# Performance work log

Measured on AMD Instinct MI355X. Metric: run time of the kernel, lower is better.

Reference implementation:

```python
import jax, jax.numpy as jnp
import numpy as np

N_NODES = 100000
N_EDGES = 800000
IN_DIM, HID_DIM, OUT_DIM = 128, 256, 128


def setup_inputs() -> dict:
    key = jax.random.key(0)
    ks = jax.random.split(key, 8)
    x = jax.random.normal(ks[0], (N_NODES, IN_DIM), dtype=jnp.float32)
    edge_index = jax.random.randint(ks[1], (2, N_EDGES), 0, N_NODES, dtype=jnp.int32)
    s = lambda k, shp, fan_in: jax.random.normal(k, shp, dtype=jnp.float32) / np.sqrt(fan_in)
    return {
        "x": x,
        "edge_index": edge_index,
        "W1_l": s(ks[2], (HID_DIM, IN_DIM), IN_DIM),   # applied to aggregated neighbors
        "b1": jnp.zeros((HID_DIM,), jnp.float32),
        "W1_r": s(ks[3], (HID_DIM, IN_DIM), IN_DIM),   # root/self transform (no bias, as in PyG)
        "W2_l": s(ks[4], (OUT_DIM, HID_DIM), HID_DIM),
        "b2": jnp.zeros((OUT_DIM,), jnp.float32),
        "W2_r": s(ks[5], (OUT_DIM, HID_DIM), HID_DIM),
    }


def _sage_conv(x, src, dst, W_l, b, W_r):
    # mean aggregation of source-neighbor features onto targets
    msg = x[src]                                              # [E, d]
    agg = jax.ops.segment_sum(msg, dst, num_segments=N_NODES)  # [N, d]
    cnt = jax.ops.segment_sum(jnp.ones((src.shape[0],), x.dtype), dst, num_segments=N_NODES)
    mean = agg / jnp.maximum(cnt, 1.0)[:, None]
    # SAGEConv: lin_l(aggr) + lin_r(x)
    return mean @ W_l.T + b + x @ W_r.T


def reference(x, edge_index, W1_l, b1, W1_r, W2_l, b2, W2_r):
    src, dst = edge_index[0], edge_index[1]
    h = jax.nn.relu(_sage_conv(x, src, dst, W1_l, b1, W1_r))
    # dropout p=0.0 -> identity (eval-mode equivalent)
    out = _sage_conv(h, src, dst, W2_l, b2, W2_r)
    return out
```

## Files before the change

kernel.cpp:

```cpp
#include <hip/hip_runtime.h>

#define NN 100000
#define NE 800000

typedef __attribute__((ext_vector_type(4))) float f32x4;
typedef __attribute__((ext_vector_type(4))) int   i32x4;
typedef __attribute__((ext_vector_type(8))) unsigned short u16x8;

__device__ __forceinline__ unsigned short f2bf(float f) {
  unsigned u = __float_as_uint(f);
  return (unsigned short)((u + 0x7FFFu + ((u >> 16) & 1u)) >> 16);
}
__device__ __forceinline__ float bf2f(unsigned short b) {
  return __uint_as_float(((unsigned)b) << 16);
}

#define NBDEG 3125
#define NXV   (NN * 128 / 4)
#define NBX   12500
#define NBW   512
__global__ __launch_bounds__(256) void prep_k(
    const float* __restrict__ x,
    const float* __restrict__ Wa, const float* __restrict__ Wbm,
    const float* __restrict__ Wc, const float* __restrict__ Wd,
    const int* __restrict__ dst,
    unsigned short* __restrict__ xb, unsigned short* __restrict__ Wbo,
    int* __restrict__ deg, int* __restrict__ rord) {
  int bid = blockIdx.x, t = threadIdx.x;
  if (bid < NBDEG) {
    int e = bid * 256 + t;
    int o = atomicAdd(&deg[dst[e]], 1);
    __builtin_nontemporal_store(o, &rord[e]);
  } else if (bid < NBDEG + NBX) {
    int i = (bid - NBDEG) * 256 + t;
    float4 v = *reinterpret_cast<const float4*>(x + (size_t)i * 4);
    ushort4 o;
    o.x = f2bf(v.x); o.y = f2bf(v.y); o.z = f2bf(v.z); o.w = f2bf(v.w);
    *reinterpret_cast<ushort4*>(xb + (size_t)i * 4) = o;
  } else {
    int k = (bid - NBDEG - NBX) * 256 + t;
    int seg = k >> 15, off = k & 32767;
    const float* s = (seg < 2) ? (seg == 0 ? Wa : Wbm) : (seg == 2 ? Wc : Wd);
    Wbo[k] = f2bf(s[off]);
  }
}

__global__ __launch_bounds__(256) void scan1_k(const int* __restrict__ deg,
    int* __restrict__ offs, int* __restrict__ bsum, float* __restrict__ inv) {
  __shared__ int s[256];
  int t = threadIdx.x;
  int base = blockIdx.x * 1024 + t * 4;
  int v[4], tsum = 0;
#pragma unroll
  for (int k = 0; k < 4; ++k) {
    int i = base + k;
    v[k] = (i < NN) ? deg[i] : 0;
    tsum += v[k];
    if (i < NN) inv[i] = 1.0f / fmaxf((float)v[k], 1.0f);
  }
  s[t] = tsum; __syncthreads();
  int val = tsum;
#pragma unroll
  for (int off = 1; off < 256; off <<= 1) {
    int x = (t >= off) ? s[t - off] : 0;
    __syncthreads();
    val += x; s[t] = val;
    __syncthreads();
  }
  int excl = val - tsum;
  if (t == 255) bsum[blockIdx.x] = val;
  int run = excl;
#pragma unroll
  for (int k = 0; k < 4; ++k) { int i = base + k; if (i < NN) offs[i] = run; run += v[k]; }
}

__global__ __launch_bounds__(256) void scan2_k(int* __restrict__ bsum, int nb) {
  __shared__ int s[256];
  int t = threadIdx.x;
  int v = (t < nb) ? bsum[t] : 0;
  s[t] = v; __syncthreads();
  int val = v;
#pragma unroll
  for (int off = 1; off < 256; off <<= 1) {
    int x = (t >= off) ? s[t - off] : 0;
    __syncthreads();
    val += x; s[t] = val;
    __syncthreads();
  }
  if (t < nb) bsum[t] = val - v;
}

#define NBFIN 98
__global__ __launch_bounds__(256) void finfill_k(
    const int* __restrict__ offs, const int* __restrict__ bsum,
    int* __restrict__ offs2,
    const int* __restrict__ src, const int* __restrict__ dst,
    const int* __restrict__ rord, int* __restrict__ eidx) {
  int bid = blockIdx.x, t = threadIdx.x;
  if (bid < NBFIN) {
    int base = bid * 1024 + t * 4;
    int add = bsum[bid];
#pragma unroll
    for (int k = 0; k < 4; ++k) {
      int i = base + k;
      if (i < NN) offs2[i] = offs[i] + add;
    }
  } else {
    int e = (bid - NBFIN) * 256 + t;
    if (e < NE) {
      int d = dst[e];
      int p = offs[d] + bsum[d >> 10] + rord[e];
      __builtin_nontemporal_store(src[e], &eidx[p]);
    }
  }
}

template<int GMODE>
__global__ __launch_bounds__(256) void gather_k(const unsigned short* __restrict__ feat,
    const int* __restrict__ offs, const int* __restrict__ deg,
    const float* __restrict__ inv, const int* __restrict__ eidx,
    const unsigned short* __restrict__ selfb,
    unsigned short* __restrict__ outb, float* __restrict__ outf) {
  const int l = threadIdx.x & 15;
  for (int nb = blockIdx.x * 16; nb < NN; nb += gridDim.x * 16) {
    int node = nb + (threadIdx.x >> 4);
    if (node >= NN) continue;
    int st = offs[node], n = deg[node];
    float a[8];
#pragma unroll
    for (int k = 0; k < 8; ++k) a[k] = 0.f;

    int j = 0;
    for (; j + 8 <= n; j += 8) {
      int si[8];
#pragma unroll
      for (int q = 0; q < 8; ++q) si[q] = eidx[st + j + q];
      u16x8 r[8];
#pragma unroll
      for (int q = 0; q < 8; ++q)
        r[q] = *reinterpret_cast<const u16x8*>(feat + (size_t)si[q] * 128 + l * 8);
#pragma unroll
      for (int q = 0; q < 8; ++q)
#pragma unroll
        for (int k = 0; k < 8; ++k) a[k] += bf2f(r[q][k]);
    }
    for (; j + 4 <= n; j += 4) {
      int si[4];
#pragma unroll
      for (int q = 0; q < 4; ++q) si[q] = eidx[st + j + q];
      u16x8 r[4];
#pragma unroll
      for (int q = 0; q < 4; ++q)
        r[q] = *reinterpret_cast<const u16x8*>(feat + (size_t)si[q] * 128 + l * 8);
#pragma unroll
      for (int q = 0; q < 4; ++q)
#pragma unroll
        for (int k = 0; k < 8; ++k) a[k] += bf2f(r[q][k]);
    }
    for (; j < n; ++j) {
      int s = eidx[st + j];
      u16x8 r = *reinterpret_cast<const u16x8*>(feat + (size_t)s * 128 + l * 8);
#pragma unroll
      for (int k = 0; k < 8; ++k) a[k] += bf2f(r[k]);
    }

    float sc = inv[node];
    if (GMODE == 2) {
      u16x8 sb = *reinterpret_cast<const u16x8*>(selfb + (size_t)node * 128 + l * 8);
      f32x4 o0, o1;
      o0[0] = bf2f(sb[0]) + sc * a[0]; o0[1] = bf2f(sb[1]) + sc * a[1];
      o0[2] = bf2f(sb[2]) + sc * a[2]; o0[3] = bf2f(sb[3]) + sc * a[3];
      o1[0] = bf2f(sb[4]) + sc * a[4]; o1[1] = bf2f(sb[5]) + sc * a[5];
      o1[2] = bf2f(sb[6]) + sc * a[6]; o1[3] = bf2f(sb[7]) + sc * a[7];
      float* po = outf + (size_t)node * 128 + l * 8;
      __builtin_nontemporal_store(o0, reinterpret_cast<f32x4*>(po));
      __builtin_nontemporal_store(o1, reinterpret_cast<f32x4*>(po + 4));
    } else {
      u16x8 o;
#pragma unroll
      for (int k = 0; k < 8; ++k) o[k] = f2bf(sc * a[k]);
      *reinterpret_cast<u16x8*>(outb + (size_t)node * 128 + l * 8) = o;
    }
  }
}

template<int MODE>
__global__ __launch_bounds__(256, 2) void mgemm_k(
    const unsigned short* __restrict__ A1, const unsigned short* __restrict__ A2,
    const unsigned short* __restrict__ Wbase, const float* __restrict__ bias,
    unsigned short* __restrict__ outb, unsigned short* __restrict__ outb2) {
  __shared__ unsigned short As[2][64 * 256];
  const int t = threadIdx.x;
  const int wave = t >> 6, lane = t & 63;
  const int lhi = lane >> 4, llo = lane & 15;

  i32x4 bfrag[8][4];
  float bv[4];
#pragma unroll
  for (int fn = 0; fn < 4; ++fn) {
    int c = wave * 64 + fn * 16 + llo;
    const unsigned short* rowp;
    if (MODE == 0) {
      rowp = Wbase + (size_t)c * 128;
      bv[fn] = bias[c];
    } else {
      rowp = Wbase + (wave >= 2 ? 32768 : 0) + (size_t)(c & 127) * 256;
      bv[fn] = (wave >= 2) ? bias[c & 127] : 0.f;
    }
#pragma unroll
    for (int ks = 0; ks < 8; ++ks) {
      int koff = (MODE == 0) ? ((ks & 3) * 32 + lhi * 8 + ((ks >= 4) ? 32768 : 0))
                             : (ks * 32 + lhi * 8);
      bfrag[ks][fn] = *reinterpret_cast<const i32x4*>(rowp + koff);
    }
  }

  auto stage = [&](int buf, int row0) {
#pragma unroll
    for (int c = 0; c < 8; ++c) {
      int chunk = wave * 8 + c;
      int tb = chunk * 1024 + lane * 16;
      int r = tb >> 9;
      int cb = tb & 511;
      int cbs = cb ^ ((r & 7) << 4);
      int gr = min(row0 + r, NN - 1);
      const char* gsrc;
      if (MODE == 0) {
        const unsigned short* Asel = (cbs < 256) ? A1 : A2;
        gsrc = (const char*)(Asel + (size_t)gr * 128) + (cbs & 255);
      } else {
        gsrc = (const char*)(A1 + (size_t)gr * 256) + cbs;
      }
      __builtin_amdgcn_global_load_lds(
          (const __attribute__((address_space(1))) void*)gsrc,
          (__attribute__((address_space(3))) void*)((char*)As + buf * 32768 + chunk * 1024),
          16, 0, 0);
    }
  };

  const int npan = (NN + 63) >> 6;
  int p = blockIdx.x;
  stage(0, p * 64);
  int cur = 0;

#pragma unroll 1
  for (; p < npan; p += gridDim.x) {
    int pn = p + gridDim.x;
    if (pn < npan) stage(cur ^ 1, pn * 64);
    asm volatile("s_waitcnt vmcnt(8)" ::: "memory");
    __builtin_amdgcn_s_barrier();

    const int row0 = p * 64;
    f32x4 acc[4][4];
#pragma unroll
    for (int fm = 0; fm < 4; ++fm)
#pragma unroll
      for (int fn = 0; fn < 4; ++fn) acc[fm][fn] = (f32x4)0.f;

#pragma unroll
    for (int ks = 0; ks < 8; ++ks) {
      i32x4 a[4];
#pragma unroll
      for (int fm = 0; fm < 4; ++fm) {
        int r = fm * 16 + llo;
        int cb = (ks * 64 + lhi * 16) ^ ((r & 7) << 4);
        a[fm] = *reinterpret_cast<const i32x4*>((const char*)As + cur * 32768 + r * 512 + cb);
      }
#pragma unroll
      for (int fm = 0; fm < 4; ++fm)
#pragma unroll
        for (int fn = 0; fn < 4; ++fn)
          asm("v_mfma_f32_16x16x32_bf16 %0, %1, %2, %0"
              : "+v"(acc[fm][fn]) : "v"(a[fm]), "v"(bfrag[ks][fn]));
    }

    asm volatile("s_nop 7\n\ts_nop 7");

#pragma unroll
    for (int fm = 0; fm < 4; ++fm) {
#pragma unroll
      for (int fn = 0; fn < 4; ++fn) {
        int col = wave * 64 + fn * 16 + llo;
#pragma unroll
        for (int j = 0; j < 4; ++j) {
          int row = row0 + fm * 16 + lhi * 4 + j;
          if (row < NN) {
            float v = acc[fm][fn][j] + bv[fn];
            if (MODE == 0) {
              v = fmaxf(v, 0.f);
              outb[(size_t)row * 256 + col] = f2bf(v);
            } else if (wave < 2) {
              outb[(size_t)row * 128 + col] = f2bf(v);
            } else {
              outb2[(size_t)row * 128 + (col - 128)] = f2bf(v);
            }
          }
        }
      }
    }
    __builtin_amdgcn_s_barrier();
    cur ^= 1;
  }
}

extern "C" void kernel_launch(void* const* d_in, const int* in_sizes, int n_in,
                              void* d_out, int out_size, void* d_ws, size_t ws_size,
                              hipStream_t stream) {
  const float* x   = (const float*)d_in[0];
  const int*   ei  = (const int*)d_in[1];
  const float* W1l = (const float*)d_in[2];
  const float* b1  = (const float*)d_in[3];
  const float* W1r = (const float*)d_in[4];
  const float* W2l = (const float*)d_in[5];
  const float* b2  = (const float*)d_in[6];
  const float* W2r = (const float*)d_in[7];
  float* out = (float*)d_out;

  char* ws = (char*)d_ws;
  float*          inv    = (float*)(ws);
  int*            deg    = (int*)(ws + 0x80000);
  int*            offs   = (int*)(ws + 0x100000);
  int*            offs2  = (int*)(ws + 0x180000);
  int*            bsum   = (int*)(ws + 0x200000);
  unsigned short* Wb     = (unsigned short*)(ws + 0x280000);
  int*            eidx   = (int*)(ws + 0x400000);
  unsigned short* xb     = (unsigned short*)(ws + 0x800000);
  unsigned short* m1b    = (unsigned short*)(ws + 0x2200000);
  unsigned short* hb     = (unsigned short*)(ws + 0x3C00000);
  unsigned short* hWb    = (unsigned short*)(ws + 0x6E00000);
  int*            rord   = (int*)(ws + 0x8600000);
  unsigned short* selfb  = m1b;

  const int* src = ei;
  const int* dst = ei + NE;
  const int NB = (NN + 1023) / 1024;

  hipMemsetAsync(deg, 0, NN * sizeof(int), stream);
  prep_k<<<NBDEG + NBX + NBW, 256, 0, stream>>>(x, W1l, W1r, W2l, W2r, dst,
                                                xb, Wb, deg, rord);
  scan1_k<<<NB, 256, 0, stream>>>(deg, offs, bsum, inv);
  scan2_k<<<1, 256, 0, stream>>>(bsum, NB);
  finfill_k<<<NBFIN + (NE + 255) / 256, 256, 0, stream>>>(offs, bsum, offs2,
                                                          src, dst, rord, eidx);

  gather_k<0><<<2048, 256, 0, stream>>>(xb, offs2, deg, inv, eidx, nullptr, m1b, nullptr);
  mgemm_k<0><<<512, 256, 0, stream>>>(m1b, xb, Wb, b1, hb, nullptr);

  mgemm_k<1><<<512, 256, 0, stream>>>(hb, nullptr, Wb + 65536, b2, hWb, selfb);
  gather_k<2><<<2048, 256, 0, stream>>>(hWb, offs2, deg, inv, eidx, selfb, nullptr, out);
}
```

Baseline: 224.9 us.

## Privatize degree counters per XCD to cut cross-die atomic contention

The degree-count atomics now go to eight separate copies of the degree array, picked by block index mod 8, which is meant to line up with the XCD round-robin block dispatch. Each edge's rank is stored together with its copy id. The scan sums the eight copies, and a new fin kernel builds per-copy offsets so edges can be scattered into CSR order. The aim is to keep atomics local to one die's L2 and avoid cross-die coherence traffic. In exchange it adds an 8x larger memset, extra reads in the scan, an extra kernel launch, and an 8*NN offset array that must be written and then read.

```diff
diff --git a/kernel.cpp b/kernel.cpp
--- a/kernel.cpp
+++ b/kernel.cpp
@@ -25,12 +25,13 @@
     const float* __restrict__ Wc, const float* __restrict__ Wd,
     const int* __restrict__ dst,
     unsigned short* __restrict__ xb, unsigned short* __restrict__ Wbo,
-    int* __restrict__ deg, int* __restrict__ rord) {
+    int* __restrict__ deg8, int* __restrict__ rord) {
   int bid = blockIdx.x, t = threadIdx.x;
   if (bid < NBDEG) {
     int e = bid * 256 + t;
-    int o = atomicAdd(&deg[dst[e]], 1);
-    __builtin_nontemporal_store(o, &rord[e]);
+    int c = bid & 7;
+    int o = atomicAdd(&deg8[c * NN + dst[e]], 1);
+    __builtin_nontemporal_store((o << 3) | c, &rord[e]);
   } else if (bid < NBDEG + NBX) {
     int i = (bid - NBDEG) * 256 + t;
     float4 v = *reinterpret_cast<const float4*>(x + (size_t)i * 4);
@@ -45,8 +46,9 @@
   }
 }
 
-__global__ __launch_bounds__(256) void scan1_k(const int* __restrict__ deg,
-    int* __restrict__ offs, int* __restrict__ bsum, float* __restrict__ inv) {
+__global__ __launch_bounds__(256) void scan1_k(const int* __restrict__ deg8,
+    int* __restrict__ degt, int* __restrict__ offs, int* __restrict__ bsum,
+    float* __restrict__ inv) {
   __shared__ int s[256];
   int t = threadIdx.x;
   int base = blockIdx.x * 1024 + t * 4;
@@ -54,9 +56,15 @@
 #pragma unroll
   for (int k = 0; k < 4; ++k) {
     int i = base + k;
-    v[k] = (i < NN) ? deg[i] : 0;
-    tsum += v[k];
-    if (i < NN) inv[i] = 1.0f / fmaxf((float)v[k], 1.0f);
+    int d = 0;
+    if (i < NN) {
+#pragma unroll
+      for (int c = 0; c < 8; ++c) d += deg8[c * NN + i];
+      degt[i] = d;
+      inv[i] = 1.0f / fmaxf((float)d, 1.0f);
+    }
+    v[k] = d;
+    tsum += d;
   }
   s[t] = tsum; __syncthreads();
   int val = tsum;
@@ -91,27 +99,36 @@
 }
 
 #define NBFIN 98
-__global__ __launch_bounds__(256) void finfill_k(
+__global__ __launch_bounds__(256) void fin_k(
     const int* __restrict__ offs, const int* __restrict__ bsum,
-    int* __restrict__ offs2,
-    const int* __restrict__ src, const int* __restrict__ dst,
-    const int* __restrict__ rord, int* __restrict__ eidx) {
-  int bid = blockIdx.x, t = threadIdx.x;
-  if (bid < NBFIN) {
-    int base = bid * 1024 + t * 4;
-    int add = bsum[bid];
-#pragma unroll
-    for (int k = 0; k < 4; ++k) {
-      int i = base + k;
-      if (i < NN) offs2[i] = offs[i] + add;
-    }
-  } else {
-    int e = (bid - NBFIN) * 256 + t;
-    if (e < NE) {
-      int d = dst[e];
-      int p = offs[d] + bsum[d >> 10] + rord[e];
-      __builtin_nontemporal_store(src[e], &eidx[p]);
-    }
+    const int* __restrict__ deg8,
+    int* __restrict__ offs2, int* __restrict__ xcdoff) {
+  int t = threadIdx.x;
+  int add = bsum[blockIdx.x];
+  int base_i = blockIdx.x * 1024 + t * 4;
+#pragma unroll
+  for (int k = 0; k < 4; ++k) {
+    int i = base_i + k;
+    if (i < NN) {
+      int run = offs[i] + add;
+      offs2[i] = run;
+#pragma unroll
+      for (int c = 0; c < 8; ++c) {
+        xcdoff[c * NN + i] = run;
+        run += deg8[c * NN + i];
+      }
+    }
+  }
+}
+
+__global__ void fill_k(const int* __restrict__ src, const int* __restrict__ dst,
+    const int* __restrict__ xcdoff, const int* __restrict__ rord,
+    int* __restrict__ eidx) {
+  int e = blockIdx.x * 256 + threadIdx.x;
+  if (e < NE) {
+    int rv = rord[e];
+    int p = xcdoff[(rv & 7) * NN + dst[e]] + (rv >> 3);
+    __builtin_nontemporal_store(src[e], &eidx[p]);
   }
 }
 
@@ -318,7 +335,7 @@
 
   char* ws = (char*)d_ws;
   float*          inv    = (float*)(ws);
-  int*            deg    = (int*)(ws + 0x80000);
+  int*            degt   = (int*)(ws + 0x80000);
   int*            offs   = (int*)(ws + 0x100000);
   int*            offs2  = (int*)(ws + 0x180000);
   int*            bsum   = (int*)(ws + 0x200000);
@@ -329,23 +346,25 @@
   unsigned short* hb     = (unsigned short*)(ws + 0x3C00000);
   unsigned short* hWb    = (unsigned short*)(ws + 0x6E00000);
   int*            rord   = (int*)(ws + 0x8600000);
+  int*            deg8   = (int*)(ws + 0x8A00000);
+  int*            xcdoff = (int*)(ws + 0x8E00000);
   unsigned short* selfb  = m1b;
 
   const int* src = ei;
   const int* dst = ei + NE;
   const int NB = (NN + 1023) / 1024;
 
-  hipMemsetAsync(deg, 0, NN * sizeof(int), stream);
+  hipMemsetAsync(deg8, 0, 8 * NN * sizeof(int), stream);
   prep_k<<<NBDEG + NBX + NBW, 256, 0, stream>>>(x, W1l, W1r, W2l, W2r, dst,
-                                                xb, Wb, deg, rord);
-  scan1_k<<<NB, 256, 0, stream>>>(deg, offs, bsum, inv);
+                                                xb, Wb, deg8, rord);
+  scan1_k<<<NB, 256, 0, stream>>>(deg8, degt, offs, bsum, inv);
   scan2_k<<<1, 256, 0, stream>>>(bsum, NB);
-  finfill_k<<<NBFIN + (NE + 255) / 256, 256, 0, stream>>>(offs, bsum, offs2,
-                                                          src, dst, rord, eidx);
-
-  gather_k<0><<<2048, 256, 0, stream>>>(xb, offs2, deg, inv, eidx, nullptr, m1b, nullptr);
+  fin_k<<<NBFIN, 256, 0, stream>>>(offs, bsum, deg8, offs2, xcdoff);
+  fill_k<<<(NE + 255) / 256, 256, 0, stream>>>(src, dst, xcdoff, rord, eidx);
+
+  gather_k<0><<<2048, 256, 0, stream>>>(xb, offs2, degt, inv, eidx, nullptr, m1b, nullptr);
   mgemm_k<0><<<512, 256, 0, stream>>>(m1b, xb, Wb, b1, hb, nullptr);
 
   mgemm_k<1><<<512, 256, 0, stream>>>(hb, nullptr, Wb + 65536, b2, hWb, selfb);
-  gather_k<2><<<2048, 256, 0, stream>>>(hWb, offs2, deg, inv, eidx, selfb, nullptr, out);
-}
+  gather_k<2><<<2048, 256, 0, stream>>>(hWb, offs2, degt, inv, eidx, selfb, nullptr, out);
+}
```

After: 229.8 us. 1.02x slower.
